# Optimization experiments

Hardware: AMD Instinct MI355X
Metric: run time of the kernel (lower is better)

The kernel has to match this reference:

```python
import jax, jax.numpy as jnp
import numpy as np

B, T, E, H = 8, 2048, 1024, 128

def setup_inputs() -> dict:
    key = jax.random.key(0)
    kx, kq, kk, kv = jax.random.split(key, 4)
    return {
        "X": jax.random.normal(kx, (B, T, E), dtype=jnp.float32),
        "Wq": jax.random.normal(kq, (E, H), dtype=jnp.float32) * (E ** -0.5),
        "Wk": jax.random.normal(kk, (E, H), dtype=jnp.float32) * (E ** -0.5),
        "Wv": jax.random.normal(kv, (E, H), dtype=jnp.float32) * (E ** -0.5),
    }

def reference(X, Wq, Wk, Wv):
    # X: [B, T, E]; Wq/Wk/Wv: [E, H]
    q = X @ Wq  # [B, T, H]
    k = X @ Wk  # [B, T, H]
    v = X @ Wv  # [B, T, H]
    t = X.shape[1]
    scale = float(X.shape[-1]) ** 0.5  # NOTE: source scales by sqrt(embedding_size)
    w = jnp.einsum("bqh,bkh->bqk", q, k) / scale  # [B, T, T]
    mask = jnp.tril(jnp.ones((t, t), dtype=bool))  # causal tril buffer
    w = jnp.where(mask[None, :, :], w, -jnp.inf)
    # NOTE: source applies softmax over dim=1 (the query axis), faithfully reproduced
    w = jax.nn.softmax(w, axis=1)
    # dropout p=0.0 -> identity
    return jnp.einsum("bqk,bkh->bqh", w, v)  # [B, T, H]
```

## Files before the change

### kernel.cpp

```cpp
#include <hip/hip_runtime.h>
#include <hip/hip_bf16.h>
#include <stdint.h>

#define B_ 8
#define T_ 2048
#define E_ 1024
#define H_ 128
#define BT_ (B_*T_)

typedef unsigned short u16;
typedef unsigned int u32;
typedef __attribute__((ext_vector_type(4))) unsigned short u16x4;
typedef __attribute__((ext_vector_type(8))) short short8;
typedef __attribute__((ext_vector_type(4))) float f32x4;

#define MFMA_BF16(a,b,c) __builtin_amdgcn_mfma_f32_16x16x32_bf16((a),(b),(c),0,0,0)

__device__ __forceinline__ u16 bf16u(float f) {
  union { float f; unsigned u; } v; v.f = f;
  unsigned r = v.u + 0x7FFFu + ((v.u >> 16) & 1u);
  return (u16)(r >> 16);
}
__device__ __forceinline__ float ubf16(u16 u) {
  union { unsigned u; float f; } v; v.u = ((unsigned)u) << 16; return v.f;
}

__device__ __forceinline__ void gl16(const void* g, void* l) {
  __builtin_amdgcn_global_load_lds(
      (const __attribute__((address_space(1))) void*)g,
      (__attribute__((address_space(3))) void*)l, 16, 0, 0);
}

template<int R, int CB, bool SWZ>
__device__ __forceinline__ void stage_tile(const char* g, int gstride, char* lds) {
  const int lane = threadIdx.x & 63;
  const int wid  = threadIdx.x >> 6;
  constexpr int LPR   = CB / 16;
  constexpr int RPC   = 1024 / CB;
  constexpr int CALLS = (R * CB) / 1024;
  constexpr int CPW   = CALLS / 4;
#pragma unroll
  for (int c = 0; c < CPW; ++c) {
    const int call = wid * CPW + c;
    const int r0   = call * RPC;
    const int row  = r0 + lane / LPR;
    int s = lane % LPR;
    if (SWZ) s = s ^ (row & 7);
    gl16(g + (size_t)row * gstride + s * 16, lds + (size_t)r0 * CB);
  }
}

__device__ __forceinline__ short8 fragr(const u16* lds, int row, int colu16, int CBu) {
  const int slot = (colu16 >> 3) ^ (row & 7);
  return *(const short8*)&lds[(size_t)row * CBu + (slot << 3)];
}

__global__ void k_prep(const float* __restrict__ X, u16* __restrict__ Xb,
                       const float* __restrict__ Wq, const float* __restrict__ Wk,
                       const float* __restrict__ Wv, u16* __restrict__ Wt) {
  const int gidx = blockIdx.x * 256 + threadIdx.x;
  const int n4 = BT_ * E_ / 4;
  for (int i = gidx; i < n4; i += gridDim.x * 256) {
    float4 v = ((const float4*)X)[i];
    u16x4 o;
    o.x = bf16u(v.x); o.y = bf16u(v.y); o.z = bf16u(v.z); o.w = bf16u(v.w);
    ((u16x4*)Xb)[i] = o;
  }
  if (gidx < 384 * 1024) {
    int r = gidx >> 10;
    int e = gidx & 1023;
    int i = r >> 7;
    int h = r & 127;
    const float* W = (i == 0) ? Wq : (i == 1) ? Wk : Wv;
    float v = W[(size_t)e * 128 + h];
    if (i == 0) v *= 0.03125f;
    Wt[gidx] = bf16u(v);
  }
}

__global__ __launch_bounds__(256) void k_qkv_gemm(const u16* __restrict__ Xb, const u16* __restrict__ Wt,
                                                  u16* __restrict__ Qs, u16* __restrict__ Kb,
                                                  u16* __restrict__ Vt) {
  __shared__ __align__(16) u16 As[128 * 64];
  __shared__ __align__(16) u16 Bs[128 * 64];
  const int m0   = blockIdx.x * 128;
  const int nsel = blockIdx.y;
  const int n0   = nsel * 128;
  const int lane = threadIdx.x & 63;
  const int wid  = threadIdx.x >> 6;
  const int ln = lane & 15, h4 = lane >> 4;
  const int wm = (wid >> 1) * 64, wn = (wid & 1) * 64;
  f32x4 acc[4][4] = {};
  for (int ks = 0; ks < E_; ks += 64) {
    stage_tile<128, 128, true>((const char*)(Xb + (size_t)m0 * E_ + ks), E_ * 2, (char*)As);
    stage_tile<128, 128, true>((const char*)(Wt + (size_t)n0 * E_ + ks), E_ * 2, (char*)Bs);
    __syncthreads();
#pragma unroll
    for (int kk = 0; kk < 2; ++kk) {
      short8 a[4], b[4];
#pragma unroll
      for (int mf = 0; mf < 4; ++mf)
        a[mf] = fragr(As, wm + mf * 16 + ln, kk * 32 + h4 * 8, 64);
#pragma unroll
      for (int nf = 0; nf < 4; ++nf)
        b[nf] = fragr(Bs, wn + nf * 16 + ln, kk * 32 + h4 * 8, 64);
#pragma unroll
      for (int mf = 0; mf < 4; ++mf)
#pragma unroll
        for (int nf = 0; nf < 4; ++nf)
          acc[mf][nf] = MFMA_BF16(a[mf], b[nf], acc[mf][nf]);
    }
    __syncthreads();
  }
#pragma unroll
  for (int mf = 0; mf < 4; ++mf)
#pragma unroll
    for (int nf = 0; nf < 4; ++nf)
#pragma unroll
      for (int i = 0; i < 4; ++i) {
        int r = m0 + wm + mf * 16 + h4 * 4 + i;
        int c = wn + nf * 16 + ln;
        u16 u = bf16u(acc[mf][nf][i]);
        if (nsel == 0)      Qs[(size_t)r * H_ + c] = u;
        else if (nsel == 1) Kb[(size_t)r * H_ + c] = u;
        else {
          int bb = r >> 11, t = r & (T_ - 1);
          Vt[((size_t)bb * H_ + c) * T_ + t] = u;
        }
      }
}

__global__ __launch_bounds__(256) void k_score(const u16* __restrict__ Qs, const u16* __restrict__ Kb,
                                               u16* __restrict__ P, float* __restrict__ colsum) {
  __shared__ __align__(16) u16 Qb[128 * 128];
  __shared__ __align__(16) u16 Kf[128 * 128];
  const int c = blockIdx.x, a = blockIdx.y, b = blockIdx.z;
  const int lo = (c * 17) >> 3, hi = ((c + 1) * 17) >> 3;
  const int lane = threadIdx.x & 63, wid = threadIdx.x >> 6;
  const int ln = lane & 15, h4 = lane >> 4;
  const int wq0 = wid * 32;
  const bool evenlane = !(ln & 1);
  int curqt = -1;
  for (int t = lo; t < hi; ++t) {
    const int qt = (t <= a) ? a : 15 - a;
    const int kt = (t <= a) ? t : t - (a + 1);
    if (qt != curqt) {
      stage_tile<128, 256, true>((const char*)(Qs + ((size_t)b * T_ + qt * 128) * H_), H_ * 2, (char*)Qb);
      curqt = qt;
    }
    stage_tile<128, 256, true>((const char*)(Kb + ((size_t)b * T_ + kt * 128) * H_), H_ * 2, (char*)Kf);
    __syncthreads();

    f32x4 acc[2][8] = {};
#pragma unroll
    for (int kk = 0; kk < 4; ++kk) {
      short8 av[2], bv[8];
#pragma unroll
      for (int mf = 0; mf < 2; ++mf)
        av[mf] = fragr(Qb, wq0 + mf * 16 + ln, kk * 32 + h4 * 8, 128);
#pragma unroll
      for (int nf = 0; nf < 8; ++nf)
        bv[nf] = fragr(Kf, nf * 16 + ln, kk * 32 + h4 * 8, 128);
#pragma unroll
      for (int mf = 0; mf < 2; ++mf)
#pragma unroll
        for (int nf = 0; nf < 8; ++nf)
          acc[mf][nf] = MFMA_BF16(av[mf], bv[nf], acc[mf][nf]);
    }

    const bool diag = (qt == kt);
#pragma unroll
    for (int nf = 0; nf < 8; ++nf) {
      float s = 0.f;
      const int k = nf * 16 + ln;
#pragma unroll
      for (int mf = 0; mf < 2; ++mf) {
#pragma unroll
        for (int i = 0; i < 4; ++i) {
          const int q = wq0 + mf * 16 + h4 * 4 + i;
          float w = __expf(acc[mf][nf][i]);
          if (diag && q < k) w = 0.f;
          acc[mf][nf][i] = w;
          s += w;
        }
      }
      s += __shfl_xor(s, 16);
      s += __shfl_xor(s, 32);
      if (h4 == 0) atomicAdd(&colsum[(size_t)b * T_ + kt * 128 + nf * 16 + ln], s);
    }
    __syncthreads();

#pragma unroll
    for (int mf = 0; mf < 2; ++mf)
#pragma unroll
      for (int nf = 0; nf < 8; ++nf) {
        f32x4 v = acc[mf][nf];
        f32x4 pv;
#pragma unroll
        for (int i = 0; i < 4; ++i) pv[i] = __shfl_xor(v[i], 1);
#pragma unroll
        for (int j = 0; j < 2; ++j) {
          const int i = evenlane ? j : (2 + j);
          const float flo = evenlane ? v[i] : pv[i];
          const float fhh = evenlane ? pv[i] : v[i];
          const u32 pk = (u32)bf16u(flo) | ((u32)bf16u(fhh) << 16);
          const int row = wq0 + mf * 16 + h4 * 4 + i;
          const int kc  = nf * 16 + (ln & ~1);
          const int byt = row * 256 + ((((kc >> 3) ^ (row & 7)) << 4) | ((kc & 7) << 1));
          *(u32*)((char*)Kf + byt) = pk;
        }
      }
    __syncthreads();

    u16* ptile = P + (((size_t)b * 136 + (size_t)qt * (qt + 1) / 2 + kt) << 14);
#pragma unroll
    for (int pass = 0; pass < 8; ++pass) {
      const int row = pass * 16 + (threadIdx.x >> 4);
      const int s   = threadIdx.x & 15;
      short8 val = *(const short8*)&Kf[row * 128 + ((s ^ (row & 7)) << 3)];
      *(short8*)&ptile[row * 128 + s * 8] = val;
    }
    __syncthreads();
  }
}

__global__ void k_finalize_v(const float* __restrict__ colsum, u16* __restrict__ Vt) {
  const int i8 = blockIdx.x * 256 + threadIdx.x;
  const int b  = i8 >> 15;
  const int r  = i8 & 32767;
  const int h  = r >> 8;
  const int t8 = r & 255;
  u16* p = Vt + ((size_t)b * H_ + h) * T_ + t8 * 8;
  const float* csp = colsum + (size_t)b * T_ + t8 * 8;
  short8 v = *(short8*)p;
  short8 o;
#pragma unroll
  for (int j = 0; j < 8; ++j) {
    float f = ubf16((u16)v[j]) / csp[j];
    o[j] = (short)bf16u(f);
  }
  *(short8*)p = o;
}

__global__ __launch_bounds__(256) void k_pv(const u16* __restrict__ P, const u16* __restrict__ Vt,
                                            float* __restrict__ out) {
  __shared__ __align__(16) u16 Pt[128 * 128];
  __shared__ __align__(16) u16 Vs[16 * 128];
  const int id = blockIdx.x;
  const int hq = id >> 6;
  const int b  = (id >> 3) & 7;
  const int a  = id & 7;
  const int lane = threadIdx.x & 63, wid = threadIdx.x >> 6;
  const int ln = lane & 15, h4 = lane >> 4;
  const int wq0 = wid * 32;
#pragma unroll
  for (int half = 0; half < 2; ++half) {
    const int qt = half ? (15 - a) : a;
    f32x4 acc[2] = {};
    for (int kt = 0; kt <= qt; ++kt) {
      const u16* ptile = P + (((size_t)b * 136 + (size_t)qt * (qt + 1) / 2 + kt) << 14);
      stage_tile<128, 256, true>((const char*)ptile, 256, (char*)Pt);
      stage_tile<16, 256, true>((const char*)(Vt + ((size_t)b * H_ + hq * 16) * T_ + kt * 128), T_ * 2, (char*)Vs);
      __syncthreads();
#pragma unroll
      for (int kk = 0; kk < 4; ++kk) {
        short8 bv = fragr(Vs, ln, kk * 32 + h4 * 8, 128);
#pragma unroll
        for (int mf = 0; mf < 2; ++mf) {
          short8 av = fragr(Pt, wq0 + mf * 16 + ln, kk * 32 + h4 * 8, 128);
          acc[mf] = MFMA_BF16(av, bv, acc[mf]);
        }
      }
      __syncthreads();
    }
#pragma unroll
    for (int mf = 0; mf < 2; ++mf)
#pragma unroll
      for (int i = 0; i < 4; ++i) {
        const int q = qt * 128 + wq0 + mf * 16 + h4 * 4 + i;
        out[((size_t)b * T_ + q) * H_ + hq * 16 + ln] = acc[mf][i];
      }
  }
}

extern "C" void kernel_launch(void* const* d_in, const int* in_sizes, int n_in,
                              void* d_out, int out_size, void* d_ws, size_t ws_size,
                              hipStream_t stream) {
  const float* X  = (const float*)d_in[0];
  const float* Wq = (const float*)d_in[1];
  const float* Wk = (const float*)d_in[2];
  const float* Wv = (const float*)d_in[3];
  float* out = (float*)d_out;
  char* ws = (char*)d_ws;

  u16 *Xb, *Wt, *Qs, *Kb, *Vt, *Pb;
  float* colsum;
  if (ws_size >= 82640896ULL) {
    Xb = (u16*)(ws + 0);
    Wt = (u16*)(ws + 33554432);
    Qs = (u16*)(ws + 34340864);
    Kb = (u16*)(ws + 38535168);
    Vt = (u16*)(ws + 42729472);
    colsum = (float*)(ws + 46923776);
    Pb = (u16*)(ws + 46989312);
  } else {
    Qs = (u16*)(ws + 0);
    Kb = (u16*)(ws + 4194304);
    Vt = (u16*)(ws + 8388608);
    colsum = (float*)(ws + 12582912);
    Pb = (u16*)(ws + 12648448);
    Xb = (u16*)(ws + 12648448);
    Wt = (u16*)(ws + 46202880);
  }

  hipMemsetAsync(colsum, 0, BT_ * sizeof(float), stream);
  k_prep<<<2048, 256, 0, stream>>>(X, Xb, Wq, Wk, Wv, Wt);
  k_qkv_gemm<<<dim3(128, 3), 256, 0, stream>>>(Xb, Wt, Qs, Kb, Vt);
  k_score<<<dim3(8, 8, 8), 256, 0, stream>>>(Qs, Kb, Pb, colsum);
  k_finalize_v<<<1024, 256, 0, stream>>>(colsum, Vt);
  k_pv<<<512, 256, 0, stream>>>(Pb, Vt, out);
}
```

Measured before the change: 180.9 us.

## Double-buffer GEMM and PV loads, keep Q in registers, drop memset

The QKV GEMM and PV kernels now use two LDS buffers, so the next tile's global-to-LDS load is issued before computing on the current one, with explicit vmcnt waits and scheduling barriers. The PV kernel flattens its two query-tile passes into one 17-step pipelined loop. The score kernel keeps its Q fragments in registers instead of LDS and writes P straight to global memory, dropping the LDS round trip and two barriers. The colsum memset is folded into the prep kernel to save a launch. In exchange, hand-tuned vmcnt counts and direct unswizzled 4-byte global stores risk correctness or coalescing problems.

```diff
diff --git a/kernel.cpp b/kernel.cpp
--- a/kernel.cpp
+++ b/kernel.cpp
@@ -15,6 +15,9 @@
 typedef __attribute__((ext_vector_type(4))) float f32x4;
 
 #define MFMA_BF16(a,b,c) __builtin_amdgcn_mfma_f32_16x16x32_bf16((a),(b),(c),0,0,0)
+
+#define SBAR() do { __builtin_amdgcn_sched_barrier(0); __builtin_amdgcn_s_barrier(); __builtin_amdgcn_sched_barrier(0); } while(0)
+#define WAITL0() asm volatile("s_waitcnt lgkmcnt(0)" ::: "memory")
 
 __device__ __forceinline__ u16 bf16u(float f) {
   union { float f; unsigned u; } v; v.f = f;
@@ -57,7 +60,8 @@
 
 __global__ void k_prep(const float* __restrict__ X, u16* __restrict__ Xb,
                        const float* __restrict__ Wq, const float* __restrict__ Wk,
-                       const float* __restrict__ Wv, u16* __restrict__ Wt) {
+                       const float* __restrict__ Wv, u16* __restrict__ Wt,
+                       float* __restrict__ colsum) {
   const int gidx = blockIdx.x * 256 + threadIdx.x;
   const int n4 = BT_ * E_ / 4;
   for (int i = gidx; i < n4; i += gridDim.x * 256) {
@@ -66,6 +70,7 @@
     o.x = bf16u(v.x); o.y = bf16u(v.y); o.z = bf16u(v.z); o.w = bf16u(v.w);
     ((u16x4*)Xb)[i] = o;
   }
+  if (gidx < BT_) colsum[gidx] = 0.f;
   if (gidx < 384 * 1024) {
     int r = gidx >> 10;
     int e = gidx & 1023;
@@ -81,8 +86,8 @@
 __global__ __launch_bounds__(256) void k_qkv_gemm(const u16* __restrict__ Xb, const u16* __restrict__ Wt,
                                                   u16* __restrict__ Qs, u16* __restrict__ Kb,
                                                   u16* __restrict__ Vt) {
-  __shared__ __align__(16) u16 As[128 * 64];
-  __shared__ __align__(16) u16 Bs[128 * 64];
+  __shared__ __align__(16) u16 As[2][128 * 64];
+  __shared__ __align__(16) u16 Bs[2][128 * 64];
   const int m0   = blockIdx.x * 128;
   const int nsel = blockIdx.y;
   const int n0   = nsel * 128;
@@ -91,26 +96,35 @@
   const int ln = lane & 15, h4 = lane >> 4;
   const int wm = (wid >> 1) * 64, wn = (wid & 1) * 64;
   f32x4 acc[4][4] = {};
-  for (int ks = 0; ks < E_; ks += 64) {
-    stage_tile<128, 128, true>((const char*)(Xb + (size_t)m0 * E_ + ks), E_ * 2, (char*)As);
-    stage_tile<128, 128, true>((const char*)(Wt + (size_t)n0 * E_ + ks), E_ * 2, (char*)Bs);
-    __syncthreads();
+
+  auto stage = [&](int t, int buf) {
+    stage_tile<128, 128, true>((const char*)(Xb + (size_t)m0 * E_ + t * 64), E_ * 2, (char*)As[buf]);
+    stage_tile<128, 128, true>((const char*)(Wt + (size_t)n0 * E_ + t * 64), E_ * 2, (char*)Bs[buf]);
+  };
+  stage(0, 0);
+  for (int t = 0; t < 16; ++t) {
+    const int cur = t & 1;
+    if (t < 15) stage(t + 1, cur ^ 1);
+    if (t < 15) asm volatile("s_waitcnt vmcnt(8)" ::: "memory");
+    else        asm volatile("s_waitcnt vmcnt(0)" ::: "memory");
+    SBAR();
 #pragma unroll
     for (int kk = 0; kk < 2; ++kk) {
       short8 a[4], b[4];
 #pragma unroll
       for (int mf = 0; mf < 4; ++mf)
-        a[mf] = fragr(As, wm + mf * 16 + ln, kk * 32 + h4 * 8, 64);
+        a[mf] = fragr(As[cur], wm + mf * 16 + ln, kk * 32 + h4 * 8, 64);
 #pragma unroll
       for (int nf = 0; nf < 4; ++nf)
-        b[nf] = fragr(Bs, wn + nf * 16 + ln, kk * 32 + h4 * 8, 64);
+        b[nf] = fragr(Bs[cur], wn + nf * 16 + ln, kk * 32 + h4 * 8, 64);
 #pragma unroll
       for (int mf = 0; mf < 4; ++mf)
 #pragma unroll
         for (int nf = 0; nf < 4; ++nf)
           acc[mf][nf] = MFMA_BF16(a[mf], b[nf], acc[mf][nf]);
     }
-    __syncthreads();
+    WAITL0();
+    SBAR();
   }
 #pragma unroll
   for (int mf = 0; mf < 4; ++mf)
@@ -124,15 +138,14 @@
         if (nsel == 0)      Qs[(size_t)r * H_ + c] = u;
         else if (nsel == 1) Kb[(size_t)r * H_ + c] = u;
         else {
-          int bb = r >> 11, t = r & (T_ - 1);
-          Vt[((size_t)bb * H_ + c) * T_ + t] = u;
+          int bb = r >> 11, tt = r & (T_ - 1);
+          Vt[((size_t)bb * H_ + c) * T_ + tt] = u;
         }
       }
 }
 
 __global__ __launch_bounds__(256) void k_score(const u16* __restrict__ Qs, const u16* __restrict__ Kb,
                                                u16* __restrict__ P, float* __restrict__ colsum) {
-  __shared__ __align__(16) u16 Qb[128 * 128];
   __shared__ __align__(16) u16 Kf[128 * 128];
   const int c = blockIdx.x, a = blockIdx.y, b = blockIdx.z;
   const int lo = (c * 17) >> 3, hi = ((c + 1) * 17) >> 3;
@@ -141,31 +154,32 @@
   const int wq0 = wid * 32;
   const bool evenlane = !(ln & 1);
   int curqt = -1;
+  short8 qa[2][4];
   for (int t = lo; t < hi; ++t) {
     const int qt = (t <= a) ? a : 15 - a;
     const int kt = (t <= a) ? t : t - (a + 1);
+    stage_tile<128, 256, true>((const char*)(Kb + ((size_t)b * T_ + kt * 128) * H_), H_ * 2, (char*)Kf);
     if (qt != curqt) {
-      stage_tile<128, 256, true>((const char*)(Qs + ((size_t)b * T_ + qt * 128) * H_), H_ * 2, (char*)Qb);
+#pragma unroll
+      for (int mf = 0; mf < 2; ++mf)
+#pragma unroll
+        for (int kk = 0; kk < 4; ++kk)
+          qa[mf][kk] = *(const short8*)&Qs[((size_t)b * T_ + qt * 128 + wq0 + mf * 16 + ln) * H_ + kk * 32 + h4 * 8];
       curqt = qt;
     }
-    stage_tile<128, 256, true>((const char*)(Kb + ((size_t)b * T_ + kt * 128) * H_), H_ * 2, (char*)Kf);
-    __syncthreads();
+    asm volatile("s_waitcnt vmcnt(0)" ::: "memory");
+    SBAR();
 
     f32x4 acc[2][8] = {};
 #pragma unroll
     for (int kk = 0; kk < 4; ++kk) {
-      short8 av[2], bv[8];
-#pragma unroll
-      for (int mf = 0; mf < 2; ++mf)
-        av[mf] = fragr(Qb, wq0 + mf * 16 + ln, kk * 32 + h4 * 8, 128);
-#pragma unroll
-      for (int nf = 0; nf < 8; ++nf)
-        bv[nf] = fragr(Kf, nf * 16 + ln, kk * 32 + h4 * 8, 128);
-#pragma unroll
-      for (int mf = 0; mf < 2; ++mf)
-#pragma unroll
-        for (int nf = 0; nf < 8; ++nf)
-          acc[mf][nf] = MFMA_BF16(av[mf], bv[nf], acc[mf][nf]);
+#pragma unroll
+      for (int nf = 0; nf < 8; ++nf) {
+        short8 bv = fragr(Kf, nf * 16 + ln, kk * 32 + h4 * 8, 128);
+#pragma unroll
+        for (int mf = 0; mf < 2; ++mf)
+          acc[mf][nf] = MFMA_BF16(qa[mf][kk], bv, acc[mf][nf]);
+      }
     }
 
     const bool diag = (qt == kt);
@@ -188,39 +202,29 @@
       s += __shfl_xor(s, 32);
       if (h4 == 0) atomicAdd(&colsum[(size_t)b * T_ + kt * 128 + nf * 16 + ln], s);
     }
-    __syncthreads();
-
+
+    u16* ptile = P + (((size_t)b * 136 + (size_t)qt * (qt + 1) / 2 + kt) << 14);
 #pragma unroll
     for (int mf = 0; mf < 2; ++mf)
 #pragma unroll
       for (int nf = 0; nf < 8; ++nf) {
         f32x4 v = acc[mf][nf];
-        f32x4 pv;
-#pragma unroll
-        for (int i = 0; i < 4; ++i) pv[i] = __shfl_xor(v[i], 1);
+        f32x4 pv_;
+#pragma unroll
+        for (int i = 0; i < 4; ++i) pv_[i] = __shfl_xor(v[i], 1);
 #pragma unroll
         for (int j = 0; j < 2; ++j) {
           const int i = evenlane ? j : (2 + j);
-          const float flo = evenlane ? v[i] : pv[i];
-          const float fhh = evenlane ? pv[i] : v[i];
+          const float flo = evenlane ? v[i] : pv_[i];
+          const float fhh = evenlane ? pv_[i] : v[i];
           const u32 pk = (u32)bf16u(flo) | ((u32)bf16u(fhh) << 16);
           const int row = wq0 + mf * 16 + h4 * 4 + i;
           const int kc  = nf * 16 + (ln & ~1);
-          const int byt = row * 256 + ((((kc >> 3) ^ (row & 7)) << 4) | ((kc & 7) << 1));
-          *(u32*)((char*)Kf + byt) = pk;
+          *(u32*)((char*)ptile + row * 256 + kc * 2) = pk;
         }
       }
-    __syncthreads();
-
-    u16* ptile = P + (((size_t)b * 136 + (size_t)qt * (qt + 1) / 2 + kt) << 14);
-#pragma unroll
-    for (int pass = 0; pass < 8; ++pass) {
-      const int row = pass * 16 + (threadIdx.x >> 4);
-      const int s   = threadIdx.x & 15;
-      short8 val = *(const short8*)&Kf[row * 128 + ((s ^ (row & 7)) << 3)];
-      *(short8*)&ptile[row * 128 + s * 8] = val;
-    }
-    __syncthreads();
+    WAITL0();
+    SBAR();
   }
 }
 
@@ -244,8 +248,8 @@
 
 __global__ __launch_bounds__(256) void k_pv(const u16* __restrict__ P, const u16* __restrict__ Vt,
                                             float* __restrict__ out) {
-  __shared__ __align__(16) u16 Pt[128 * 128];
-  __shared__ __align__(16) u16 Vs[16 * 128];
+  __shared__ __align__(16) u16 Pt[2][128 * 128];
+  __shared__ __align__(16) u16 Vs[2][16 * 128];
   const int id = blockIdx.x;
   const int hq = id >> 6;
   const int b  = (id >> 3) & 7;
@@ -253,33 +257,46 @@
   const int lane = threadIdx.x & 63, wid = threadIdx.x >> 6;
   const int ln = lane & 15, h4 = lane >> 4;
   const int wq0 = wid * 32;
-#pragma unroll
-  for (int half = 0; half < 2; ++half) {
-    const int qt = half ? (15 - a) : a;
-    f32x4 acc[2] = {};
-    for (int kt = 0; kt <= qt; ++kt) {
-      const u16* ptile = P + (((size_t)b * 136 + (size_t)qt * (qt + 1) / 2 + kt) << 14);
-      stage_tile<128, 256, true>((const char*)ptile, 256, (char*)Pt);
-      stage_tile<16, 256, true>((const char*)(Vt + ((size_t)b * H_ + hq * 16) * T_ + kt * 128), T_ * 2, (char*)Vs);
-      __syncthreads();
-#pragma unroll
-      for (int kk = 0; kk < 4; ++kk) {
-        short8 bv = fragr(Vs, ln, kk * 32 + h4 * 8, 128);
-#pragma unroll
-        for (int mf = 0; mf < 2; ++mf) {
-          short8 av = fragr(Pt, wq0 + mf * 16 + ln, kk * 32 + h4 * 8, 128);
-          acc[mf] = MFMA_BF16(av, bv, acc[mf]);
+
+  auto stage = [&](int t, int buf) {
+    const int qt = (t <= a) ? a : 15 - a;
+    const int kt = (t <= a) ? t : t - (a + 1);
+    const u16* ptile = P + (((size_t)b * 136 + (size_t)qt * (qt + 1) / 2 + kt) << 14);
+    stage_tile<128, 256, true>((const char*)ptile, 256, (char*)Pt[buf]);
+    stage_tile<16, 256, true>((const char*)(Vt + ((size_t)b * H_ + hq * 16) * T_ + kt * 128), T_ * 2, (char*)Vs[buf]);
+  };
+
+  stage(0, 0);
+  f32x4 acc[2] = {};
+  for (int t = 0; t < 17; ++t) {
+    const int cur = t & 1;
+    if (t < 16) stage(t + 1, cur ^ 1);
+    if (t < 16) asm volatile("s_waitcnt vmcnt(9)" ::: "memory");
+    else        asm volatile("s_waitcnt vmcnt(0)" ::: "memory");
+    SBAR();
+#pragma unroll
+    for (int kk = 0; kk < 4; ++kk) {
+      short8 bv = fragr(Vs[cur], ln, kk * 32 + h4 * 8, 128);
+#pragma unroll
+      for (int mf = 0; mf < 2; ++mf) {
+        short8 av = fragr(Pt[cur], wq0 + mf * 16 + ln, kk * 32 + h4 * 8, 128);
+        acc[mf] = MFMA_BF16(av, bv, acc[mf]);
+      }
+    }
+    if (t == a || t == 16) {
+      const int qt = (t == a) ? a : 15 - a;
+#pragma unroll
+      for (int mf = 0; mf < 2; ++mf) {
+#pragma unroll
+        for (int i = 0; i < 4; ++i) {
+          const int q = qt * 128 + wq0 + mf * 16 + h4 * 4 + i;
+          out[((size_t)b * T_ + q) * H_ + hq * 16 + ln] = acc[mf][i];
         }
-      }
-      __syncthreads();
-    }
-#pragma unroll
-    for (int mf = 0; mf < 2; ++mf)
-#pragma unroll
-      for (int i = 0; i < 4; ++i) {
-        const int q = qt * 128 + wq0 + mf * 16 + h4 * 4 + i;
-        out[((size_t)b * T_ + q) * H_ + hq * 16 + ln] = acc[mf][i];
-      }
+        acc[mf] = (f32x4){0.f, 0.f, 0.f, 0.f};
+      }
+    }
+    WAITL0();
+    SBAR();
   }
 }
 
@@ -313,8 +330,7 @@
     Wt = (u16*)(ws + 46202880);
   }
 
-  hipMemsetAsync(colsum, 0, BT_ * sizeof(float), stream);
-  k_prep<<<2048, 256, 0, stream>>>(X, Xb, Wq, Wk, Wv, Wt);
+  k_prep<<<2048, 256, 0, stream>>>(X, Xb, Wq, Wk, Wv, Wt, colsum);
   k_qkv_gemm<<<dim3(128, 3), 256, 0, stream>>>(Xb, Wt, Qs, Kb, Vt);
   k_score<<<dim3(8, 8, 8), 256, 0, stream>>>(Qs, Kb, Pb, colsum);
   k_finalize_v<<<1024, 256, 0, stream>>>(colsum, Vt);
```

Result: no change. 180.0 us (-0.5%).
